# Performance work log

Measured on AMD Instinct MI355X. Metric: run time of the kernel, lower is better.

The kernel has to match this reference:

```python
import jax, jax.numpy as jnp
import numpy as np

B, CIN, HIN, WIN = 2, 128, 91, 180
COUT, HOUT, WOUT = 64, 181, 360
K = 9                      # number of DISCO basis functions (3x3 kernel_shape)
NNZ = HOUT * WOUT * 8      # ~8 sparse basis entries per output point
CTOT = 128
GROUPS = 8
NHEADS = 4
EPS = 1e-5


def group_norm(x, gamma, beta, groups):
    b, c, h, w = x.shape
    xg = x.reshape(b, groups, c // groups, h, w)
    mu = xg.mean(axis=(2, 3, 4), keepdims=True)
    var = xg.var(axis=(2, 3, 4), keepdims=True)
    xn = ((xg - mu) * jax.lax.rsqrt(var + EPS)).reshape(b, c, h, w)
    return xn * gamma[None, :, None, None] + beta[None, :, None, None]


def setup_inputs() -> dict:
    key = jax.random.key(0)
    ks = jax.random.split(key, 12)
    x = jax.random.normal(ks[0], (B, CIN, HIN, WIN), jnp.float32)
    skip = jax.random.normal(ks[1], (B, CTOT - COUT, HOUT, WOUT), jnp.float32)
    # DISCO transpose conv params: per-basis channel mixing weight + bias
    w_disco = jax.random.normal(ks[2], (COUT, CIN, K), jnp.float32) * (1.0 / np.sqrt(CIN * K))
    b_disco = jnp.zeros((COUT,), jnp.float32)
    # precomputed sparse basis (COO): value, output point, input point, basis index
    psi_val = jax.random.uniform(ks[3], (NNZ,), jnp.float32)
    row_idx = jax.random.randint(ks[4], (NNZ,), 0, HOUT * WOUT)
    col_idx = jax.random.randint(ks[5], (NNZ,), 0, HIN * WIN)
    ker_idx = jax.random.randint(ks[6], (NNZ,), 0, K)
    # quadrature weights per input latitude
    quad = jax.random.uniform(ks[7], (HIN,), jnp.float32, 0.5, 1.5) * (np.pi / HIN)
    g1 = jnp.ones((COUT,), jnp.float32); b1 = jnp.zeros((COUT,), jnp.float32)
    g2 = jnp.ones((CTOT,), jnp.float32); b2 = jnp.zeros((CTOT,), jnp.float32)
    wqkv = jax.random.normal(ks[8], (CTOT, 3 * CTOT), jnp.float32) * (1.0 / np.sqrt(CTOT))
    bqkv = jnp.zeros((3 * CTOT,), jnp.float32)
    wo = jax.random.normal(ks[9], (CTOT, CTOT), jnp.float32) * (1.0 / np.sqrt(CTOT))
    bo = jnp.zeros((CTOT,), jnp.float32)
    return dict(x=x, skip=skip, w_disco=w_disco, b_disco=b_disco, psi_val=psi_val,
                quad=quad, g1=g1, b1=b1, g2=g2, b2=b2, wqkv=wqkv, bqkv=bqkv,
                wo=wo, bo=bo, row_idx=row_idx, col_idx=col_idx, ker_idx=ker_idx)


def reference(x, skip, w_disco, b_disco, psi_val, quad, g1, b1, g2, b2,
              wqkv, bqkv, wo, bo, row_idx, col_idx, ker_idx):
    b, cin, hin, win = x.shape
    hout, wout = skip.shape[2], skip.shape[3]
    # ---- DISCO transpose conv: quadrature weight, channel mix per basis, sparse scatter ----
    xq = (x * quad[None, None, :, None]).reshape(b, cin, hin * win)          # [B,Cin,Nin]
    xw = jnp.einsum('bcn,ock->bokn', xq, w_disco)                            # [B,Cout,K,Nin]
    gathered = psi_val[None, None, :] * xw[:, :, ker_idx, col_idx]           # [B,Cout,NNZ]
    y = jnp.zeros((b, COUT, hout * wout), x.dtype).at[:, :, row_idx].add(gathered)
    y = y.reshape(b, COUT, hout, wout) + b_disco[None, :, None, None]
    # ---- norm + GELU (exact erf, matching torch default) ----
    y = jax.nn.gelu(group_norm(y, g1, b1, GROUPS), approximate=False)
    # ---- concat skip ----
    h = jnp.concatenate([y, skip], axis=1)                                   # [B,CTOT,Hout,Wout]
    # ---- FlowerBlock: groupnorm + MHA along longitude per latitude ring, residual outside ----
    t = group_norm(h, g2, b2, GROUPS).transpose(0, 2, 3, 1)                  # [B,H,W,C]
    qkv = t @ wqkv + bqkv
    q, k, v = jnp.split(qkv, 3, axis=-1)
    hd = CTOT // NHEADS
    def heads(a):
        return a.reshape(b, hout, wout, NHEADS, hd).transpose(0, 1, 3, 2, 4)  # [B,H,nh,W,hd]
    q, k, v = heads(q), heads(k), heads(v)
    scores = jnp.einsum('bhnqd,bhnkd->bhnqk', q, k) * (1.0 / np.sqrt(hd))
    attn = jax.nn.softmax(scores, axis=-1)
    o = jnp.einsum('bhnqk,bhnkd->bhnqd', attn, v)
    o = o.transpose(0, 1, 3, 2, 4).reshape(b, hout, wout, CTOT)
    o = (o @ wo + bo).transpose(0, 3, 1, 2)                                  # [B,C,H,W]
    return o + h
```

## Files before the change

### kernel.cpp

```cpp
#include <hip/hip_runtime.h>
#include <hip/hip_bf16.h>

#define B_ 2
#define CIN 128
#define HIN 91
#define WIN 180
#define NIN (HIN*WIN)
#define COUT_ 64
#define HOUT 181
#define WOUT 360
#define NOUT (HOUT*WOUT)
#define KK 9
#define NNZ_ (NOUT*8)
#define CTOT 128
#define NH 4
#define HD 32
#define EPS_ 1e-5f
#define PTOT ((size_t)B_*NOUT)
#define BCAP 40

#define QSCALE (0.17677669529663688f * 1.4426950408889634f)

typedef short s16x8 __attribute__((ext_vector_type(8)));
typedef float f32x4v __attribute__((ext_vector_type(4)));
typedef float f32x16v __attribute__((ext_vector_type(16)));
typedef int i32x2v __attribute__((ext_vector_type(2)));

#define OFF_Q  ((size_t)0)
#define OFF_K  ((size_t)8340480)
#define OFF_WOT ((size_t)16680960)
#define OFF_H  ((size_t)18869760)
#define OFF_S1 (OFF_H + (size_t)B_*NOUT*CTOT)
#define OFF_S2 (OFF_S1 + 32)
#define OFF_WT (OFF_S2 + 32)
#define OFF_VT (OFF_WT + (size_t)KK*CIN*COUT_)
#define OFF_CNT OFF_VT
#define OFF_CSR (OFF_VT + 65536)

__device__ inline ushort f2b(float x) { return __bfloat16_as_ushort(__float2bfloat16(x)); }
__device__ inline float b2f(ushort u) { return __bfloat162float(__ushort_as_bfloat16(u)); }
__device__ inline uint pk2(float lo, float hi) {
    return (uint)f2b(lo) | ((uint)f2b(hi) << 16);
}

__global__ __launch_bounds__(256) void kT(const float* __restrict__ wd, const float* __restrict__ wqkv,
                                          const float* __restrict__ wo, ushort* __restrict__ wtb,
                                          ushort* __restrict__ wqt, ushort* __restrict__ wot) {
    int idx = blockIdx.x * 256 + threadIdx.x;
    if (idx < KK * CIN * COUT_) {
        int cin = idx & 127;
        int rest = idx >> 7;
        int cout = rest & 63;
        int k = rest >> 6;
        wtb[idx] = f2b(wd[((size_t)cout * CIN + cin) * KK + k]);
    } else if (idx < KK * CIN * COUT_ + 384 * 128) {
        int i2 = idx - KK * CIN * COUT_;
        int n = i2 >> 7, kk = i2 & 127;
        float v = wqkv[(size_t)kk * 384 + n];
        if (n < 128) v *= QSCALE;
        wqt[i2] = f2b(v);
    } else {
        int i3 = idx - (KK * CIN * COUT_ + 384 * 128);
        if (i3 < 128 * 128) {
            int n = i3 >> 7, kk = i3 & 127;
            wot[i3] = f2b(wo[(size_t)kk * 128 + n]);
        }
    }
}

#define KA_BLOCKS 256
__global__ __launch_bounds__(256) void kAF(const float* __restrict__ x, const ushort* __restrict__ wtb,
                                           const float* __restrict__ quad, ushort* __restrict__ xw,
                                           const int* __restrict__ row, const int* __restrict__ col,
                                           const int* __restrict__ ker, const float* __restrict__ psi,
                                           int* __restrict__ cnt, uint2* __restrict__ csr) {
    __shared__ ushort As[128][128];
    __shared__ __align__(16) char buf[16384];
    int tid = threadIdx.x;
    if (blockIdx.x >= KA_BLOCKS) {
        int e = (blockIdx.x - KA_BLOCKS) * 256 + tid;
        if (e < NNZ_) {
            int r = row[e];
            int pos = atomicAdd(&cnt[r], 1);
            if (pos < BCAP) {
                uint2 pl;
                pl.x = (uint)col[e] | ((uint)ker[e] << 20);
                pl.y = __float_as_uint(psi[e]);
                csr[(size_t)r * BCAP + pos] = pl;
            }
        }
        return;
    }
    ushort (*Bs)[128] = reinterpret_cast<ushort(*)[128]>(buf);
    ushort (*Bo)[64]  = reinterpret_cast<ushort(*)[64]>(buf);
    float  (*tmp)[17] = reinterpret_cast<float(*)[17]>(buf);
    int n0 = (blockIdx.x & 127) * 128;
    int b  = blockIdx.x >> 7;
    const float* xb = x + (size_t)b * CIN * NIN;
    for (int s = 0; s < 8; ++s) {
        int nbase = n0 + s * 16;
        for (int idx = tid; idx < 128 * 16; idx += 256) {
            int cin = idx >> 4, nn = idx & 15;
            int n = nbase + nn;
            tmp[cin][nn] = (n < NIN) ? xb[(size_t)cin * NIN + n] : 0.f;
        }
        __syncthreads();
        {
            int rl = tid >> 4, c8 = tid & 15;
            int n = nbase + rl;
            float qd = (n < NIN) ? quad[n / WIN] : 0.f;
            ushort w8[8];
            #pragma unroll
            for (int i = 0; i < 8; ++i) w8[i] = f2b(tmp[c8 * 8 + i][rl] * qd);
            int rowi = s * 16 + rl;
            *reinterpret_cast<uint4*>(&As[rowi][(c8 ^ (rowi & 7)) * 8]) = *reinterpret_cast<const uint4*>(w8);
        }
        __syncthreads();
    }
    int w = tid >> 6, lane = tid & 63;
    int l16 = lane & 15, kh = lane >> 4;
    int sa = l16 & 7;
    for (int k = 0; k < KK; ++k) {
        __syncthreads();
        for (int i = tid; i < 1024; i += 256) {
            int rl = i >> 4, c8 = i & 15;
            uint4 v = *reinterpret_cast<const uint4*>(wtb + (((size_t)k * 64 + rl) << 7) + c8 * 8);
            *reinterpret_cast<uint4*>(&Bs[rl][(c8 ^ (rl & 7)) * 8]) = v;
        }
        __syncthreads();
        f32x4v acc[2][4];
        #pragma unroll
        for (int mi = 0; mi < 2; ++mi)
            #pragma unroll
            for (int nf = 0; nf < 4; ++nf) { acc[mi][nf][0] = 0; acc[mi][nf][1] = 0; acc[mi][nf][2] = 0; acc[mi][nf][3] = 0; }
        #pragma unroll
        for (int ks = 0; ks < 4; ++ks) {
            int c8 = ks * 4 + kh;
            s16x8 a0 = *reinterpret_cast<const s16x8*>(&As[w * 32 + l16][(c8 ^ sa) * 8]);
            s16x8 a1 = *reinterpret_cast<const s16x8*>(&As[w * 32 + 16 + l16][(c8 ^ sa) * 8]);
            #pragma unroll
            for (int nf = 0; nf < 4; ++nf) {
                int nn = nf * 16 + l16;
                s16x8 bf = *reinterpret_cast<const s16x8*>(&Bs[nn][(c8 ^ (nn & 7)) * 8]);
                acc[0][nf] = __builtin_amdgcn_mfma_f32_16x16x32_bf16(a0, bf, acc[0][nf], 0, 0, 0);
                acc[1][nf] = __builtin_amdgcn_mfma_f32_16x16x32_bf16(a1, bf, acc[1][nf], 0, 0, 0);
            }
        }
        __syncthreads();
        #pragma unroll
        for (int mi = 0; mi < 2; ++mi) {
            #pragma unroll
            for (int nf = 0; nf < 4; ++nf) {
                int coli = nf * 16 + l16;
                #pragma unroll
                for (int j = 0; j < 4; ++j) {
                    int rowl = w * 32 + mi * 16 + kh * 4 + j;
                    Bo[rowl][((coli >> 3) ^ (rowl & 7)) * 8 + (coli & 7)] = f2b(acc[mi][nf][j]);
                }
            }
        }
        __syncthreads();
        for (int i = tid; i < 1024; i += 256) {
            int rl = i >> 3, u = i & 7;
            int n = n0 + rl;
            if (n < NIN) {
                uint4 v = *reinterpret_cast<const uint4*>(&Bo[rl][(u ^ (rl & 7)) * 8]);
                *reinterpret_cast<uint4*>(xw + (((size_t)(k * NIN + n) * 2 + b) << 6) + u * 8) = v;
            }
        }
    }
}

#define SKIP_BLOCKS 1024
#define GGRID 2037
__global__ __launch_bounds__(256) void kGS(const uint* __restrict__ xw, const int* __restrict__ cnt,
                                           const uint2* __restrict__ csr, ushort* __restrict__ h16,
                                           const float* __restrict__ bd, float* __restrict__ s1,
                                           const float* __restrict__ skip, float* __restrict__ s2) {
    __shared__ float tile[32][33];
    __shared__ float acc4[4];
    __shared__ float red[4][2][8][2];
    int tid = threadIdx.x;
    uint* hw = reinterpret_cast<uint*>(h16);
    if (blockIdx.x < SKIP_BLOCKS) {
        int bx = blockIdx.x & 255;
        int c0 = ((blockIdx.x >> 8) & 1) * 32;
        int b  = blockIdx.x >> 9;
        int tx = tid & 31, ty = tid >> 5;
        if (tid < 4) acc4[tid] = 0.f;
        float sA[2] = {0.f, 0.f}, qA[2] = {0.f, 0.f};
        for (int n0 = bx * 32; n0 < NOUT; n0 += 256 * 32) {
            #pragma unroll
            for (int j = 0; j < 4; ++j) {
                int c = c0 + ty + j * 8, n = n0 + tx;
                if (n < NOUT) {
                    float v = skip[((size_t)b * 64 + c) * NOUT + n];
                    tile[ty + j * 8][tx] = v;
                    int gi = (ty + 8 * j) >> 4;
                    sA[gi] += v; qA[gi] += v * v;
                }
            }
            __syncthreads();
            for (int idx = tid; idx < 512; idx += 256) {
                int nn = idx >> 4, cp = idx & 15;
                int n = n0 + nn;
                if (n < NOUT) {
                    uint st = pk2(tile[cp * 2][nn], tile[cp * 2 + 1][nn]);
                    hw[((size_t)b * NOUT + n) * 64 + 32 + (c0 >> 1) + cp] = st;
                }
            }
            __syncthreads();
        }
        atomicAdd(&acc4[0], sA[0]); atomicAdd(&acc4[1], qA[0]);
        atomicAdd(&acc4[2], sA[1]); atomicAdd(&acc4[3], qA[1]);
        __syncthreads();
        if (tid < 4) {
            int gi = tid >> 1, isq = tid & 1;
            int g = 4 + (c0 >> 4) + gi;
            atomicAdd(&s2[(b * 8 + g) * 2 + isq], acc4[tid]);
        }
        return;
    }
    int gbid = blockIdx.x - SKIP_BLOCKS;
    int lane = tid & 63;
    int wv = tid >> 6;
    int b = lane >> 5;
    int c2 = lane & 31;
    float2 bdv = *reinterpret_cast<const float2*>(&bd[c2 * 2]);
    float sA = 0.f, qA = 0.f;
    for (int r = gbid * 4 + wv; r < NOUT; r += GGRID * 4) {
        int n = min(cnt[r], BCAP);
        float a0 = 0.f, a1 = 0.f;
        const uint2* bucket = csr + (size_t)r * BCAP;
        for (int i = 0; i < n; ++i) {
            uint2 pl = bucket[i];
            int c = pl.x & 0xFFFFF;
            int kk = pl.x >> 20;
            float p = __uint_as_float(pl.y);
            uint v = xw[((size_t)kk * NIN + c) * 64 + lane];
            a0 = fmaf(p, b2f((ushort)(v & 0xFFFF)), a0);
            a1 = fmaf(p, b2f((ushort)(v >> 16)), a1);
        }
        hw[((size_t)b * NOUT + r) * 64 + c2] = pk2(a0, a1);
        float y0 = a0 + bdv.x, y1 = a1 + bdv.y;
        sA += y0 + y1; qA += y0 * y0 + y1 * y1;
    }
    #pragma unroll
    for (int o = 1; o <= 2; o <<= 1) { sA += __shfl_xor(sA, o); qA += __shfl_xor(qA, o); }
    if ((lane & 3) == 0) {
        red[wv][b][c2 >> 2][0] = sA;
        red[wv][b][c2 >> 2][1] = qA;
    }
    __syncthreads();
    if (tid < 32) {
        int bb = tid >> 4, g = (tid >> 1) & 7, isq = tid & 1;
        float v = red[0][bb][g][isq] + red[1][bb][g][isq] + red[2][bb][g][isq] + red[3][bb][g][isq];
        atomicAdd(&s1[(bb * 8 + g) * 2 + isq], v);
    }
}

#define AGRID 2048
__global__ __launch_bounds__(256) void kApply1(ushort* __restrict__ h16, const float* __restrict__ bd,
                                               const float* __restrict__ g1, const float* __restrict__ b1,
                                               const float* __restrict__ s1, float* __restrict__ s2) {
    int tid = threadIdx.x;
    int c8g = tid & 7;
    int lane = tid & 63, wv = tid >> 6;
    const float invc = 1.0f / (8.0f * NOUT);
    float mu0 = s1[c8g * 2] * invc;
    float r0 = rsqrtf(s1[c8g * 2 + 1] * invc - mu0 * mu0 + EPS_);
    float mu1 = s1[(8 + c8g) * 2] * invc;
    float r1 = rsqrtf(s1[(8 + c8g) * 2 + 1] * invc - mu1 * mu1 + EPS_);
    float bdv[8], g1v[8], b1v[8];
    #pragma unroll
    for (int j = 0; j < 8; ++j) {
        int c = c8g * 8 + j;
        bdv[j] = bd[c]; g1v[j] = g1[c]; b1v[j] = b1[c];
    }
    float sA[2] = {0.f, 0.f}, qA[2] = {0.f, 0.f};
    const size_t total = (size_t)B_ * NOUT * 8;
    uint4* hb = reinterpret_cast<uint4*>(h16);
    for (size_t idx = (size_t)blockIdx.x * 256 + tid; idx < total; idx += (size_t)AGRID * 256) {
        size_t pn = idx >> 3;
        int b = pn >= (size_t)NOUT;
        float mu = b ? mu1 : mu0, rstd = b ? r1 : r0;
        uint4* p = hb + pn * 16 + c8g;
        uint4 hv = *p;
        const ushort* hs = reinterpret_cast<const ushort*>(&hv);
        float ls = 0.f, lq = 0.f;
        uint outw[4];
        #pragma unroll
        for (int jp = 0; jp < 4; ++jp) {
            float a0 = b2f(hs[jp * 2]) + bdv[jp * 2];
            float a1 = b2f(hs[jp * 2 + 1]) + bdv[jp * 2 + 1];
            float t0 = (a0 - mu) * rstd * g1v[jp * 2] + b1v[jp * 2];
            float t1 = (a1 - mu) * rstd * g1v[jp * 2 + 1] + b1v[jp * 2 + 1];
            float ge0 = t0 * 0.5f * (1.0f + erff(t0 * 0.70710678118654752f));
            float ge1 = t1 * 0.5f * (1.0f + erff(t1 * 0.70710678118654752f));
            ls += ge0 + ge1; lq += ge0 * ge0 + ge1 * ge1;
            outw[jp] = pk2(ge0, ge1);
        }
        sA[b] += ls; qA[b] += lq;
        uint4 st = {outw[0], outw[1], outw[2], outw[3]};
        *p = st;
    }
    #pragma unroll
    for (int o = 8; o <= 32; o <<= 1) {
        sA[0] += __shfl_xor(sA[0], o); qA[0] += __shfl_xor(qA[0], o);
        sA[1] += __shfl_xor(sA[1], o); qA[1] += __shfl_xor(qA[1], o);
    }
    sA[0] += __shfl_xor(sA[0], 1); qA[0] += __shfl_xor(qA[0], 1);
    sA[1] += __shfl_xor(sA[1], 1); qA[1] += __shfl_xor(qA[1], 1);
    __shared__ float red[4][4][4];
    if (lane < 8 && !(lane & 1)) {
        int g = lane >> 1;
        red[wv][g][0] = sA[0]; red[wv][g][1] = qA[0];
        red[wv][g][2] = sA[1]; red[wv][g][3] = qA[1];
    }
    __syncthreads();
    if (tid < 16) {
        int g = tid >> 2, q = tid & 3;
        float v = red[0][g][q] + red[1][g][q] + red[2][g][q] + red[3][g][q];
        int b = q >> 1, isq = q & 1;
        atomicAdd(&s2[(b * 8 + g) * 2 + isq], v);
    }
}

__global__ __launch_bounds__(256) void kQKV(const ushort* __restrict__ h16, const ushort* __restrict__ wqt,
                                            const float* __restrict__ bqkv, const float* __restrict__ g2,
                                            const float* __restrict__ b2, const float* __restrict__ s2,
                                            ushort* __restrict__ qg, ushort* __restrict__ kg,
                                            ushort* __restrict__ vtg) {
    __shared__ ushort As[128][128];
    __shared__ ushort Bs[128][128];
    __shared__ float muT[16], rsT[16], g2T[128], b2T[128];
    int tid = threadIdx.x;
    size_t r0 = (size_t)blockIdx.x * 128;
    const float invc2 = 1.0f / (16.0f * NOUT);
    if (tid < 16) {
        float mu = s2[tid * 2] * invc2;
        float ex2 = s2[tid * 2 + 1] * invc2;
        muT[tid] = mu;
        rsT[tid] = rsqrtf(ex2 - mu * mu + EPS_);
    }
    if (tid < 128) { g2T[tid] = g2[tid]; b2T[tid] = b2[tid]; }
    __syncthreads();
    const uint4* hb = reinterpret_cast<const uint4*>(h16);
    for (int i = tid; i < 2048; i += 256) {
        int rl = i >> 4, c8 = i & 15;
        size_t rg = r0 + rl;
        uint4 wv = {0, 0, 0, 0};
        if (rg < PTOT) {
            int c = c8 * 8;
            int g = ((rg >= (size_t)NOUT) ? 8 : 0) + (c >> 4);
            float mu = muT[g], rs = rsT[g];
            uint4 hv = hb[rg * 16 + c8];
            const ushort* hs = reinterpret_cast<const ushort*>(&hv);
            float t[8];
            #pragma unroll
            for (int j = 0; j < 8; ++j)
                t[j] = (b2f(hs[j]) - mu) * rs * g2T[c + j] + b2T[c + j];
            wv.x = pk2(t[0], t[1]); wv.y = pk2(t[2], t[3]);
            wv.z = pk2(t[4], t[5]); wv.w = pk2(t[6], t[7]);
        }
        *reinterpret_cast<uint4*>(&As[rl][(c8 ^ (rl & 7)) * 8]) = wv;
    }
    int w = tid >> 6, lane = tid & 63;
    int l16 = lane & 15, kh = lane >> 4;
    int sa = l16 & 7;
    for (int n0 = 0; n0 < 384; n0 += 128) {
        __syncthreads();
        for (int i = tid; i < 2048; i += 256) {
            int rl = i >> 4, c8 = i & 15;
            uint4 v = *reinterpret_cast<const uint4*>(wqt + ((size_t)(n0 + rl) << 7) + c8 * 8);
            *reinterpret_cast<uint4*>(&Bs[rl][(c8 ^ (rl & 7)) * 8]) = v;
        }
        __syncthreads();
        f32x4v acc[2][8];
        #pragma unroll
        for (int mi = 0; mi < 2; ++mi)
            #pragma unroll
            for (int nf = 0; nf < 8; ++nf) { acc[mi][nf][0] = 0; acc[mi][nf][1] = 0; acc[mi][nf][2] = 0; acc[mi][nf][3] = 0; }
        #pragma unroll
        for (int ks = 0; ks < 4; ++ks) {
            int c8 = ks * 4 + kh;
            s16x8 a0 = *reinterpret_cast<const s16x8*>(&As[w * 32 + l16][(c8 ^ sa) * 8]);
            s16x8 a1 = *reinterpret_cast<const s16x8*>(&As[w * 32 + 16 + l16][(c8 ^ sa) * 8]);
            #pragma unroll
            for (int nf = 0; nf < 8; ++nf) {
                int nn = nf * 16 + l16;
                s16x8 bf = *reinterpret_cast<const s16x8*>(&Bs[nn][(c8 ^ (nn & 7)) * 8]);
                acc[0][nf] = __builtin_amdgcn_mfma_f32_16x16x32_bf16(a0, bf, acc[0][nf], 0, 0, 0);
                acc[1][nf] = __builtin_amdgcn_mfma_f32_16x16x32_bf16(a1, bf, acc[1][nf], 0, 0, 0);
            }
        }
        if (n0 < 256) {
            __syncthreads();
            const float bscale = (n0 == 0) ? QSCALE : 1.0f;
            #pragma unroll
            for (int mi = 0; mi < 2; ++mi) {
                #pragma unroll
                for (int nf = 0; nf < 8; ++nf) {
                    int coli = nf * 16 + l16;
                    float bias = bqkv[n0 + coli] * bscale;
                    #pragma unroll
                    for (int j = 0; j < 4; ++j) {
                        int rowl = w * 32 + mi * 16 + kh * 4 + j;
                        Bs[rowl][((coli >> 3) ^ (rowl & 7)) * 8 + (coli & 7)] = f2b(acc[mi][nf][j] + bias);
                    }
                }
            }
            __syncthreads();
            ushort* dst = (n0 == 0) ? qg : kg;
            for (int i = tid; i < 2048; i += 256) {
                int rl = i >> 4, c8 = i & 15;
                size_t rg = r0 + rl;
                if (rg < PTOT) {
                    uint4 v = *reinterpret_cast<const uint4*>(&Bs[rl][(c8 ^ (rl & 7)) * 8]);
                    *(reinterpret_cast<uint4*>(dst) + rg * 16 + c8) = v;
                }
            }
        } else {
            #pragma unroll
            for (int mi = 0; mi < 2; ++mi) {
                size_t rg0 = r0 + w * 32 + mi * 16 + kh * 4;
                if (rg0 < PTOT) {
                    int b = rg0 >= (size_t)NOUT;
                    size_t n = rg0 - (size_t)b * NOUT;
                    #pragma unroll
                    for (int nf = 0; nf < 8; ++nf) {
                        int coli = nf * 16 + l16;
                        float bias = bqkv[256 + coli];
                        uint2 st = { pk2(acc[mi][nf][0] + bias, acc[mi][nf][1] + bias),
                                     pk2(acc[mi][nf][2] + bias, acc[mi][nf][3] + bias) };
                        *reinterpret_cast<uint2*>(&vtg[((size_t)(b * 128 + coli)) * NOUT + n]) = st;
                    }
                }
            }
        }
    }
}

__global__ __launch_bounds__(384) void kAttn(const ushort* __restrict__ qg, const ushort* __restrict__ kg,
                                             const ushort* __restrict__ vtg, ushort* __restrict__ og) {
    __shared__ ushort K_sm[360][40];
    __shared__ ushort V_sm[32][392];
    int head = blockIdx.x, ring = blockIdx.y, b = blockIdx.z;
    int tid = threadIdx.x;
    size_t rowbase = (size_t)b * NOUT + (size_t)ring * 360;
    for (int i = tid; i < 1440; i += 384) {
        int r = i >> 2, c = (i & 3) * 8;
        uint4 val = *reinterpret_cast<const uint4*>(kg + (rowbase + r) * 128 + head * 32 + c);
        *reinterpret_cast<uint4*>(&K_sm[r][c]) = val;
    }
    {
        int d = tid / 12, j = tid % 12;
        const ushort* vp = vtg + ((size_t)(b * 128 + head * 32 + d)) * NOUT + (size_t)ring * 360;
        for (int c8 = j; c8 < 49; c8 += 12) {
            uint4 val = {0, 0, 0, 0};
            if (c8 < 45) val = *reinterpret_cast<const uint4*>(vp + c8 * 8);
            *reinterpret_cast<uint4*>(&V_sm[d][c8 * 8]) = val;
        }
    }
    __syncthreads();
    int wv = tid >> 6, lane = tid & 63;
    int lq = lane & 31, hi = lane >> 5;
    s16x8 qa[2], qb[2];
    bool qok[2];
    int qvv[2];
    #pragma unroll
    for (int qi = 0; qi < 2; ++qi) {
        int qt = wv + qi * 6;
        qvv[qi] = qt * 32 + lq;
        qok[qi] = qvv[qi] < 360;
        uint4 qf1 = {0, 0, 0, 0}, qf2 = {0, 0, 0, 0};
        if (qok[qi]) {
            const ushort* qp = qg + (rowbase + qvv[qi]) * 128 + head * 32;
            qf1 = *reinterpret_cast<const uint4*>(qp + hi * 8);
            qf2 = *reinterpret_cast<const uint4*>(qp + 16 + hi * 8);
        }
        qa[qi] = __builtin_bit_cast(s16x8, qf1);
        qb[qi] = __builtin_bit_cast(s16x8, qf2);
    }
    f32x16v O[2];
    #pragma unroll
    for (int qi = 0; qi < 2; ++qi)
        #pragma unroll
        for (int r2 = 0; r2 < 16; ++r2) O[qi][r2] = 0.f;
    float ls0[2] = {0.f, 0.f}, ls1[2] = {0.f, 0.f};
    #pragma unroll 1
    for (int kt = 0; kt < 12; ++kt) {
        int krow = min(kt * 32 + lq, 359);
        s16x8 ka = *reinterpret_cast<const s16x8*>(&K_sm[krow][hi * 8]);
        s16x8 kb = *reinterpret_cast<const s16x8*>(&K_sm[krow][16 + hi * 8]);
        s16x8 va = *reinterpret_cast<const s16x8*>(&V_sm[lq][kt * 32 + hi * 8]);
        s16x8 vb = *reinterpret_cast<const s16x8*>(&V_sm[lq][kt * 32 + 16 + hi * 8]);
        #pragma unroll
        for (int qi = 0; qi < 2; ++qi) {
            f32x16v S;
            #pragma unroll
            for (int r2 = 0; r2 < 16; ++r2) S[r2] = 0.f;
            S = __builtin_amdgcn_mfma_f32_32x32x16_bf16(ka, qa[qi], S, 0, 0, 0);
            S = __builtin_amdgcn_mfma_f32_32x32x16_bf16(kb, qb[qi], S, 0, 0, 0);
            if (kt == 11) {
                #pragma unroll
                for (int r2 = 4; r2 < 16; ++r2) S[r2] = -1e30f;
            }
            uint pw[8];
            #pragma unroll
            for (int pr = 0; pr < 8; ++pr) {
                float e0 = __builtin_amdgcn_exp2f(S[pr * 2]);
                float e1 = __builtin_amdgcn_exp2f(S[pr * 2 + 1]);
                pw[pr] = pk2(e0, e1);
                if (pr & 1) ls1[qi] += e0 + e1; else ls0[qi] += e0 + e1;
            }
            i32x2v r01 = __builtin_amdgcn_permlane32_swap((int)pw[0], (int)pw[2], false, false);
            i32x2v r11 = __builtin_amdgcn_permlane32_swap((int)pw[1], (int)pw[3], false, false);
            i32x2v r21 = __builtin_amdgcn_permlane32_swap((int)pw[4], (int)pw[6], false, false);
            i32x2v r31 = __builtin_amdgcn_permlane32_swap((int)pw[5], (int)pw[7], false, false);
            uint4 pf1u = {(uint)r01[0], (uint)r11[0], (uint)r01[1], (uint)r11[1]};
            uint4 pf2u = {(uint)r21[0], (uint)r31[0], (uint)r21[1], (uint)r31[1]};
            O[qi] = __builtin_amdgcn_mfma_f32_32x32x16_bf16(va, __builtin_bit_cast(s16x8, pf1u), O[qi], 0, 0, 0);
            O[qi] = __builtin_amdgcn_mfma_f32_32x32x16_bf16(vb, __builtin_bit_cast(s16x8, pf2u), O[qi], 0, 0, 0);
        }
        __builtin_amdgcn_sched_barrier(0);
    }
    #pragma unroll
    for (int qi = 0; qi < 2; ++qi) {
        float lsum = ls0[qi] + ls1[qi];
        i32x2v sw = __builtin_amdgcn_permlane32_swap(__float_as_int(lsum), __float_as_int(lsum), false, false);
        lsum = __int_as_float(sw[0]) + __int_as_float(sw[1]);
        float inv = 1.f / lsum;
        if (qok[qi]) {
            ushort* op = og + (rowbase + qvv[qi]) * 128 + head * 32;
            #pragma unroll
            for (int g4 = 0; g4 < 4; ++g4) {
                int dbase = g4 * 8 + hi * 4;
                uint w0 = pk2(O[qi][g4 * 4 + 0] * inv, O[qi][g4 * 4 + 1] * inv);
                uint w1 = pk2(O[qi][g4 * 4 + 2] * inv, O[qi][g4 * 4 + 3] * inv);
                uint2 st = {w0, w1};
                *reinterpret_cast<uint2*>(op + dbase) = st;
            }
        }
    }
}

__global__ __launch_bounds__(256) void kFinal(const ushort* __restrict__ ob, const ushort* __restrict__ wot,
                                              const float* __restrict__ bo, const ushort* __restrict__ h16,
                                              float* __restrict__ out) {
    __shared__ ushort AB[2][128][128];
    int tid = threadIdx.x;
    size_t r0 = (size_t)blockIdx.x * 128;
    for (int i = tid; i < 2048; i += 256) {
        int rl = i >> 4, c8 = i & 15;
        size_t rg = r0 + rl;
        uint4 v = {0, 0, 0, 0};
        if (rg < PTOT) v = *reinterpret_cast<const uint4*>(ob + (rg << 7) + c8 * 8);
        *reinterpret_cast<uint4*>(&AB[0][rl][(c8 ^ (rl & 7)) * 8]) = v;
    }
    for (int i = tid; i < 2048; i += 256) {
        int rl = i >> 4, c8 = i & 15;
        uint4 v = *reinterpret_cast<const uint4*>(wot + ((size_t)rl << 7) + c8 * 8);
        *reinterpret_cast<uint4*>(&AB[1][rl][(c8 ^ (rl & 7)) * 8]) = v;
    }
    __syncthreads();
    int w = tid >> 6, lane = tid & 63;
    int l16 = lane & 15, kh = lane >> 4;
    int sa = l16 & 7;
    f32x4v acc[2][8];
    #pragma unroll
    for (int mi = 0; mi < 2; ++mi)
        #pragma unroll
        for (int nf = 0; nf < 8; ++nf) { acc[mi][nf][0] = 0; acc[mi][nf][1] = 0; acc[mi][nf][2] = 0; acc[mi][nf][3] = 0; }
    #pragma unroll
    for (int ks = 0; ks < 4; ++ks) {
        int c8 = ks * 4 + kh;
        s16x8 a0 = *reinterpret_cast<const s16x8*>(&AB[0][w * 32 + l16][(c8 ^ sa) * 8]);
        s16x8 a1 = *reinterpret_cast<const s16x8*>(&AB[0][w * 32 + 16 + l16][(c8 ^ sa) * 8]);
        #pragma unroll
        for (int nf = 0; nf < 8; ++nf) {
            int nn = nf * 16 + l16;
            s16x8 bf = *reinterpret_cast<const s16x8*>(&AB[1][nn][(c8 ^ (nn & 7)) * 8]);
            acc[0][nf] = __builtin_amdgcn_mfma_f32_16x16x32_bf16(a0, bf, acc[0][nf], 0, 0, 0);
            acc[1][nf] = __builtin_amdgcn_mfma_f32_16x16x32_bf16(a1, bf, acc[1][nf], 0, 0, 0);
        }
    }
    float* trf = reinterpret_cast<float*>(&AB[0][0][0]);
    const uint* h32 = reinterpret_cast<const uint*>(h16);
    int hw = w >> 1;
    for (int half = 0; half < 2; ++half) {
        __syncthreads();
        if (hw == half) {
            #pragma unroll
            for (int mi = 0; mi < 2; ++mi) {
                #pragma unroll
                for (int nf = 0; nf < 8; ++nf) {
                    int coli = nf * 16 + l16;
                    float bv = bo[coli];
                    #pragma unroll
                    for (int j = 0; j < 4; ++j) {
                        int relrow = (w & 1) * 32 + mi * 16 + kh * 4 + j;
                        trf[relrow * 129 + coli] = acc[mi][nf][j] + bv;
                    }
                }
            }
        }
        __syncthreads();
        for (int i = tid; i < 4096; i += 256) {
            int rl = i >> 6, c2 = i & 63;
            size_t p = r0 + half * 64 + rl;
            if (p < PTOT) {
                uint hv = h32[p * 64 + c2];
                trf[rl * 129 + c2 * 2]     += b2f((ushort)(hv & 0xFFFF));
                trf[rl * 129 + c2 * 2 + 1] += b2f((ushort)(hv >> 16));
            }
        }
        __syncthreads();
        for (int i = tid; i < 8192; i += 256) {
            int c = i >> 6, rl = i & 63;
            size_t p = r0 + half * 64 + rl;
            if (p < PTOT) {
                int b = p >= (size_t)NOUT;
                size_t n = p - (size_t)b * NOUT;
                out[((size_t)(b * 128 + c)) * NOUT + n] = trf[rl * 129 + c];
            }
        }
    }
}

extern "C" void kernel_launch(void* const* d_in, const int* in_sizes, int n_in,
                              void* d_out, int out_size, void* d_ws, size_t ws_size,
                              hipStream_t stream) {
    const float* x    = (const float*)d_in[0];
    const float* skip = (const float*)d_in[1];
    const float* wd   = (const float*)d_in[2];
    const float* bd   = (const float*)d_in[3];
    const float* psi  = (const float*)d_in[4];
    const float* quad = (const float*)d_in[5];
    const float* g1   = (const float*)d_in[6];
    const float* b1   = (const float*)d_in[7];
    const float* g2   = (const float*)d_in[8];
    const float* b2   = (const float*)d_in[9];
    const float* wqkv = (const float*)d_in[10];
    const float* bqkv = (const float*)d_in[11];
    const float* wo   = (const float*)d_in[12];
    const float* bo   = (const float*)d_in[13];
    const int* row    = (const int*)d_in[14];
    const int* col    = (const int*)d_in[15];
    const int* ker    = (const int*)d_in[16];
    float* ws = (float*)d_ws;
    ushort* xw = (ushort*)ws;
    ushort* h16 = (ushort*)(ws + OFF_H);
    float* s1 = ws + OFF_S1;
    float* s2 = ws + OFF_S2;
    ushort* wtb = (ushort*)(ws + OFF_WT);
    int*   cnt = (int*)(ws + OFF_CNT);
    uint2* csr = (uint2*)(ws + OFF_CSR);
    ushort* qb  = (ushort*)(ws + OFF_Q);
    ushort* kb  = (ushort*)(ws + OFF_K);
    ushort* vtb = (ushort*)(ws + OFF_VT);
    ushort* wot = (ushort*)(ws + OFF_WOT);
    ushort* wqt = (ushort*)d_out;
    float* out = (float*)d_out;

    hipMemsetAsync(s1, 0, 64 * sizeof(float), stream);
    hipMemsetAsync(cnt, 0, 65536 * sizeof(int), stream);

    kT<<<544, 256, 0, stream>>>(wd, wqkv, wo, wtb, wqt, wot);
    kAF<<<KA_BLOCKS + 2037, 256, 0, stream>>>(x, wtb, quad, xw, row, col, ker, psi, cnt, csr);
    kGS<<<SKIP_BLOCKS + GGRID, 256, 0, stream>>>((const uint*)xw, cnt, csr, h16, bd, s1, skip, s2);
    kApply1<<<AGRID, 256, 0, stream>>>(h16, bd, g1, b1, s1, s2);
    kQKV<<<(int)((PTOT + 127) / 128), 256, 0, stream>>>(h16, wqt, bqkv, g2, b2, s2, qb, kb, vtb);
    kAttn<<<dim3(NH, HOUT, B_), 384, 0, stream>>>(qb, kb, vtb, qb );
    kFinal<<<(int)((PTOT + 127) / 128), 256, 0, stream>>>(qb, wot, bo, h16, out);
}
```

Baseline: 383.2 us.

## Move skip-channel copy into kAF and batch gather loads in kGather

The skip-tensor transpose-to-bf16 and its group-norm statistics move out of the gather kernel. They now run as extra blocks of the kAF launch, alongside the CSR fill and the input channel-mixing GEMM. The remaining gather kernel issues the first 8 bucket entries and their xw loads up front, then does the FMAs, with a scalar tail loop for longer buckets. This adds memory-level parallelism to the latency-bound sparse gather and overlaps the bandwidth-bound skip copy with compute. The cost is that padding slots beyond the count are read speculatively and redirected to a safe address.

```diff
diff --git a/kernel.cpp b/kernel.cpp
--- a/kernel.cpp
+++ b/kernel.cpp
@@ -69,16 +69,20 @@
 }
 
 #define KA_BLOCKS 256
+#define SKIP_BASE 256
+#define FILL_BASE 1280
 __global__ __launch_bounds__(256) void kAF(const float* __restrict__ x, const ushort* __restrict__ wtb,
                                            const float* __restrict__ quad, ushort* __restrict__ xw,
                                            const int* __restrict__ row, const int* __restrict__ col,
                                            const int* __restrict__ ker, const float* __restrict__ psi,
-                                           int* __restrict__ cnt, uint2* __restrict__ csr) {
+                                           int* __restrict__ cnt, uint2* __restrict__ csr,
+                                           const float* __restrict__ skip, ushort* __restrict__ h16,
+                                           float* __restrict__ s2) {
     __shared__ ushort As[128][128];
     __shared__ __align__(16) char buf[16384];
     int tid = threadIdx.x;
-    if (blockIdx.x >= KA_BLOCKS) {
-        int e = (blockIdx.x - KA_BLOCKS) * 256 + tid;
+    if (blockIdx.x >= FILL_BASE) {
+        int e = (blockIdx.x - FILL_BASE) * 256 + tid;
         if (e < NNZ_) {
             int r = row[e];
             int pos = atomicAdd(&cnt[r], 1);
@@ -88,6 +92,49 @@
                 pl.y = __float_as_uint(psi[e]);
                 csr[(size_t)r * BCAP + pos] = pl;
             }
+        }
+        return;
+    }
+    if (blockIdx.x >= SKIP_BASE) {
+        float (*tile)[33] = reinterpret_cast<float(*)[33]>(buf);
+        float* acc4 = reinterpret_cast<float*>(buf + 32 * 33 * 4);
+        int idx4 = blockIdx.x - SKIP_BASE;
+        int bx = idx4 & 255;
+        int c0 = ((idx4 >> 8) & 1) * 32;
+        int b  = idx4 >> 9;
+        int tx = tid & 31, ty = tid >> 5;
+        if (tid < 4) acc4[tid] = 0.f;
+        float sA[2] = {0.f, 0.f}, qA[2] = {0.f, 0.f};
+        uint* hw = reinterpret_cast<uint*>(h16);
+        for (int n0 = bx * 32; n0 < NOUT; n0 += 256 * 32) {
+            #pragma unroll
+            for (int j = 0; j < 4; ++j) {
+                int c = c0 + ty + j * 8, n = n0 + tx;
+                if (n < NOUT) {
+                    float v = skip[((size_t)b * 64 + c) * NOUT + n];
+                    tile[ty + j * 8][tx] = v;
+                    int gi = (ty + 8 * j) >> 4;
+                    sA[gi] += v; qA[gi] += v * v;
+                }
+            }
+            __syncthreads();
+            for (int idx = tid; idx < 512; idx += 256) {
+                int nn = idx >> 4, cp = idx & 15;
+                int n = n0 + nn;
+                if (n < NOUT) {
+                    uint st = pk2(tile[cp * 2][nn], tile[cp * 2 + 1][nn]);
+                    hw[((size_t)b * NOUT + n) * 64 + 32 + (c0 >> 1) + cp] = st;
+                }
+            }
+            __syncthreads();
+        }
+        atomicAdd(&acc4[0], sA[0]); atomicAdd(&acc4[1], qA[0]);
+        atomicAdd(&acc4[2], sA[1]); atomicAdd(&acc4[3], qA[1]);
+        __syncthreads();
+        if (tid < 4) {
+            int gi = tid >> 1, isq = tid & 1;
+            int g = 4 + (c0 >> 4) + gi;
+            atomicAdd(&s2[(b * 8 + g) * 2 + isq], acc4[tid]);
         }
         return;
     }
@@ -171,75 +218,43 @@
     }
 }
 
-#define SKIP_BLOCKS 1024
 #define GGRID 2037
-__global__ __launch_bounds__(256) void kGS(const uint* __restrict__ xw, const int* __restrict__ cnt,
-                                           const uint2* __restrict__ csr, ushort* __restrict__ h16,
-                                           const float* __restrict__ bd, float* __restrict__ s1,
-                                           const float* __restrict__ skip, float* __restrict__ s2) {
-    __shared__ float tile[32][33];
-    __shared__ float acc4[4];
-    __shared__ float red[4][2][8][2];
+__global__ __launch_bounds__(256) void kGather(const uint* __restrict__ xw, const int* __restrict__ cnt,
+                                               const uint2* __restrict__ csr, ushort* __restrict__ h16,
+                                               const float* __restrict__ bd, float* __restrict__ s1) {
     int tid = threadIdx.x;
-    uint* hw = reinterpret_cast<uint*>(h16);
-    if (blockIdx.x < SKIP_BLOCKS) {
-        int bx = blockIdx.x & 255;
-        int c0 = ((blockIdx.x >> 8) & 1) * 32;
-        int b  = blockIdx.x >> 9;
-        int tx = tid & 31, ty = tid >> 5;
-        if (tid < 4) acc4[tid] = 0.f;
-        float sA[2] = {0.f, 0.f}, qA[2] = {0.f, 0.f};
-        for (int n0 = bx * 32; n0 < NOUT; n0 += 256 * 32) {
-            #pragma unroll
-            for (int j = 0; j < 4; ++j) {
-                int c = c0 + ty + j * 8, n = n0 + tx;
-                if (n < NOUT) {
-                    float v = skip[((size_t)b * 64 + c) * NOUT + n];
-                    tile[ty + j * 8][tx] = v;
-                    int gi = (ty + 8 * j) >> 4;
-                    sA[gi] += v; qA[gi] += v * v;
-                }
-            }
-            __syncthreads();
-            for (int idx = tid; idx < 512; idx += 256) {
-                int nn = idx >> 4, cp = idx & 15;
-                int n = n0 + nn;
-                if (n < NOUT) {
-                    uint st = pk2(tile[cp * 2][nn], tile[cp * 2 + 1][nn]);
-                    hw[((size_t)b * NOUT + n) * 64 + 32 + (c0 >> 1) + cp] = st;
-                }
-            }
-            __syncthreads();
-        }
-        atomicAdd(&acc4[0], sA[0]); atomicAdd(&acc4[1], qA[0]);
-        atomicAdd(&acc4[2], sA[1]); atomicAdd(&acc4[3], qA[1]);
-        __syncthreads();
-        if (tid < 4) {
-            int gi = tid >> 1, isq = tid & 1;
-            int g = 4 + (c0 >> 4) + gi;
-            atomicAdd(&s2[(b * 8 + g) * 2 + isq], acc4[tid]);
-        }
-        return;
-    }
-    int gbid = blockIdx.x - SKIP_BLOCKS;
     int lane = tid & 63;
     int wv = tid >> 6;
     int b = lane >> 5;
     int c2 = lane & 31;
     float2 bdv = *reinterpret_cast<const float2*>(&bd[c2 * 2]);
     float sA = 0.f, qA = 0.f;
-    for (int r = gbid * 4 + wv; r < NOUT; r += GGRID * 4) {
+    uint* hw = reinterpret_cast<uint*>(h16);
+    for (int r = blockIdx.x * 4 + wv; r < NOUT; r += GGRID * 4) {
         int n = min(cnt[r], BCAP);
+        const uint2* bucket = csr + (size_t)r * BCAP;
         float a0 = 0.f, a1 = 0.f;
-        const uint2* bucket = csr + (size_t)r * BCAP;
-        for (int i = 0; i < n; ++i) {
-            uint2 pl = bucket[i];
-            int c = pl.x & 0xFFFFF;
-            int kk = pl.x >> 20;
-            float p = __uint_as_float(pl.y);
-            uint v = xw[((size_t)kk * NIN + c) * 64 + lane];
-            a0 = fmaf(p, b2f((ushort)(v & 0xFFFF)), a0);
-            a1 = fmaf(p, b2f((ushort)(v >> 16)), a1);
+        uint2 pl[8];
+        #pragma unroll
+        for (int i = 0; i < 8; ++i) pl[i] = bucket[i];
+        uint v[8];
+        #pragma unroll
+        for (int i = 0; i < 8; ++i) {
+            size_t base = ((size_t)(pl[i].x >> 20) * NIN + (pl[i].x & 0xFFFFF)) * 64 + lane;
+            v[i] = xw[(i < n) ? base : (size_t)lane];
+        }
+        #pragma unroll
+        for (int i = 0; i < 8; ++i) {
+            float p = (i < n) ? __uint_as_float(pl[i].y) : 0.f;
+            a0 = fmaf(p, b2f((ushort)(v[i] & 0xFFFF)), a0);
+            a1 = fmaf(p, b2f((ushort)(v[i] >> 16)), a1);
+        }
+        for (int i = 8; i < n; ++i) {
+            uint2 ple = bucket[i];
+            float p = __uint_as_float(ple.y);
+            uint ve = xw[((size_t)(ple.x >> 20) * NIN + (ple.x & 0xFFFFF)) * 64 + lane];
+            a0 = fmaf(p, b2f((ushort)(ve & 0xFFFF)), a0);
+            a1 = fmaf(p, b2f((ushort)(ve >> 16)), a1);
         }
         hw[((size_t)b * NOUT + r) * 64 + c2] = pk2(a0, a1);
         float y0 = a0 + bdv.x, y1 = a1 + bdv.y;
@@ -247,6 +262,7 @@
     }
     #pragma unroll
     for (int o = 1; o <= 2; o <<= 1) { sA += __shfl_xor(sA, o); qA += __shfl_xor(qA, o); }
+    __shared__ float red[4][2][8][2];
     if ((lane & 3) == 0) {
         red[wv][b][c2 >> 2][0] = sA;
         red[wv][b][c2 >> 2][1] = qA;
@@ -667,8 +683,9 @@
     hipMemsetAsync(cnt, 0, 65536 * sizeof(int), stream);
 
     kT<<<544, 256, 0, stream>>>(wd, wqkv, wo, wtb, wqt, wot);
-    kAF<<<KA_BLOCKS + 2037, 256, 0, stream>>>(x, wtb, quad, xw, row, col, ker, psi, cnt, csr);
-    kGS<<<SKIP_BLOCKS + GGRID, 256, 0, stream>>>((const uint*)xw, cnt, csr, h16, bd, s1, skip, s2);
+    kAF<<<FILL_BASE + 2037, 256, 0, stream>>>(x, wtb, quad, xw, row, col, ker, psi, cnt, csr,
+                                              skip, h16, s2);
+    kGather<<<GGRID, 256, 0, stream>>>((const uint*)xw, cnt, csr, h16, bd, s1);
     kApply1<<<AGRID, 256, 0, stream>>>(h16, bd, g1, b1, s1, s2);
     kQKV<<<(int)((PTOT + 127) / 128), 256, 0, stream>>>(h16, wqt, bqkv, g2, b2, s2, qb, kb, vtb);
     kAttn<<<dim3(NH, HOUT, B_), 384, 0, stream>>>(qb, kb, vtb, qb );
```

After: 360.7 us (median of 2 runs). 5.9% less time.
